# Kernel optimization log

Measured on AMD Instinct MI355X. Metric: run time of the kernel, lower is better.

## Reference

```python
import jax, jax.numpy as jnp
import numpy as np

N_MOLS = 2048
DEPTH = 4

def _graph_conv(fatoms, fbonds, agraph, bgraph, Wi, Wh, Wo, bo):
    # fbonds: [n_bonds, 88] -> nei_input_h: [n_bonds, H]
    nei_input_h = fbonds @ Wi.T
    msg = jax.nn.relu(nei_input_h)
    for _ in range(DEPTH - 1):
        # gather neighbor bond messages [n_bonds, max_nei, H], sum over neighbors
        nei = msg[bgraph].sum(axis=1)
        msg = jax.nn.relu(nei_input_h + nei @ Wh.T)
    # aggregate bond messages into atoms: [n_atoms, max_nei, H] -> [n_atoms, H]
    atom_nei = msg[agraph].sum(axis=1)
    atom_in = jnp.concatenate([fatoms, atom_nei], axis=1)  # [n_atoms, 82+H]
    return jax.nn.relu(atom_in @ Wo.T + bo)

def _mol_embed(atom_h, mol_idx):
    return jax.ops.segment_sum(atom_h, mol_idx, num_segments=N_MOLS)

def setup_inputs() -> dict:
    key = jax.random.key(0)
    ks = jax.random.split(key, 24)
    n_atoms, n_bonds, max_nei, H = 100000, 200000, 10, 256
    d = {}
    d['fatoms_src'] = jax.random.normal(ks[0], (n_atoms, 82), jnp.float32)
    d['fbonds_src'] = jax.random.normal(ks[1], (n_bonds, 88), jnp.float32)
    d['agraph_src'] = jax.random.randint(ks[2], (n_atoms, max_nei), 0, n_bonds, jnp.int32)
    d['bgraph_src'] = jax.random.randint(ks[3], (n_bonds, max_nei), 0, n_bonds, jnp.int32)
    d['mol_idx_src'] = jnp.sort(jax.random.randint(ks[4], (n_atoms,), 0, N_MOLS, jnp.int32))
    d['fatoms_tgt'] = jax.random.normal(ks[5], (n_atoms, 82), jnp.float32)
    d['fbonds_tgt'] = jax.random.normal(ks[6], (n_bonds, 88), jnp.float32)
    d['agraph_tgt'] = jax.random.randint(ks[7], (n_atoms, max_nei), 0, n_bonds, jnp.int32)
    d['bgraph_tgt'] = jax.random.randint(ks[8], (n_bonds, max_nei), 0, n_bonds, jnp.int32)
    d['mol_idx_tgt'] = jnp.sort(jax.random.randint(ks[9], (n_atoms,), 0, N_MOLS, jnp.int32))
    s = 0.05
    d['Wi_s'] = jax.random.normal(ks[10], (H, 88), jnp.float32) * s
    d['Wh_s'] = jax.random.normal(ks[11], (H, H), jnp.float32) * s
    d['Wo_s'] = jax.random.normal(ks[12], (H, 82 + H), jnp.float32) * s
    d['bo_s'] = jax.random.normal(ks[13], (H,), jnp.float32) * s
    d['Wi_t'] = jax.random.normal(ks[14], (H, 88), jnp.float32) * s
    d['Wh_t'] = jax.random.normal(ks[15], (H, H), jnp.float32) * s
    d['Wo_t'] = jax.random.normal(ks[16], (H, 82 + H), jnp.float32) * s
    d['bo_t'] = jax.random.normal(ks[17], (H,), jnp.float32) * s
    d['Wrh'] = jax.random.normal(ks[18], (H, H), jnp.float32) * s
    d['brh'] = jax.random.normal(ks[19], (H,), jnp.float32) * s
    d['Wro'] = jax.random.normal(ks[20], (1, H), jnp.float32) * s
    d['bro'] = jax.random.normal(ks[21], (1,), jnp.float32) * s
    return d

def reference(fatoms_src, fbonds_src, agraph_src, bgraph_src, mol_idx_src,
              fatoms_tgt, fbonds_tgt, agraph_tgt, bgraph_tgt, mol_idx_tgt,
              Wi_s, Wh_s, Wo_s, bo_s, Wi_t, Wh_t, Wo_t, bo_t,
              Wrh, brh, Wro, bro):
    src_atom_h = _graph_conv(fatoms_src, fbonds_src, agraph_src, bgraph_src, Wi_s, Wh_s, Wo_s, bo_s)
    src_mol_h = _mol_embed(src_atom_h, mol_idx_src)
    tgt_atom_h = _graph_conv(fatoms_tgt, fbonds_tgt, agraph_tgt, bgraph_tgt, Wi_t, Wh_t, Wo_t, bo_t)
    tgt_mol_h = _mol_embed(tgt_atom_h, mol_idx_tgt)
    rxn_h = jax.nn.relu((tgt_mol_h - src_mol_h) @ Wrh.T + brh)
    return rxn_h @ Wro.T + bro  # [N_MOLS, 1]
```

## Files before the change

kernel.cpp:

```cpp
#include <hip/hip_runtime.h>

typedef _Float16 f16;
using f16x8 = __attribute__((ext_vector_type(8))) _Float16;
using f32x4 = __attribute__((ext_vector_type(4))) float;

#define H 256
#define NM 2048

__device__ __forceinline__ void gload_lds16(const f16* g, f16* lds)
{
    __builtin_amdgcn_global_load_lds(
        (const __attribute__((address_space(1))) void*)g,
        (__attribute__((address_space(3))) void*)lds, 16, 0, 0);
}

__device__ __forceinline__ void gemm_body(
    f16 (*Bs)[64],
    const float* __restrict__ A1, int lda1, int K1r,
    const f16*  __restrict__ W1,
    const f16*  __restrict__ A2,
    const f16*  __restrict__ W2,
    const float* __restrict__ bias, f16* __restrict__ C,
    int bm, int Mend)
{
    const int tid  = threadIdx.x;
    const int wave = tid >> 6, lane = tid & 63;
    const int lrow = lane & 15;
    const int kg   = lane >> 4;
    const int swz  = lrow & 7;
    const int glr  = lane >> 3;
    const int gsc  = (lane & 7) ^ glr;

    const int  myrow = bm + wave * 16 + lrow;
    const bool rowok = myrow < Mend;

    f32x4 acc[16];
    #pragma unroll
    for (int n = 0; n < 16; ++n) acc[n] = (f32x4){0.f, 0.f, 0.f, 0.f};

    f16x8 af2[8];
    if (A2 != nullptr) {
        #pragma unroll
        for (int t = 0; t < 8; ++t) {
            if (rowok)
                af2[t] = *(const f16x8*)(A2 + (size_t)myrow * H + kg * 8 + t * 32);
            else {
                #pragma unroll
                for (int e = 0; e < 8; ++e) af2[t][e] = (f16)0.f;
            }
        }
    }

    auto stageB = [&](const f16* W, int ldw, int k0) {
        #pragma unroll
        for (int q = 0; q < 8; ++q)
            gload_lds16(W + (size_t)(wave * 64 + q * 8 + glr) * ldw + k0 + gsc * 8,
                        &Bs[wave * 64 + q * 8][0]);
    };

    auto mfma_win = [&](f16x8 a0, f16x8 a1) {
        #pragma unroll
        for (int ks = 0; ks < 2; ++ks) {
            const int cb = ((ks * 4 + kg) ^ swz) * 8;
            const f16x8 av = ks ? a1 : a0;
            #pragma unroll
            for (int n = 0; n < 16; ++n) {
                f16x8 b = *(const f16x8*)&Bs[n * 16 + lrow][cb];
                acc[n] = __builtin_amdgcn_mfma_f32_16x16x32_f16(av, b, acc[n], 0, 0, 0);
            }
        }
    };

    if (A1 != nullptr) {
        #pragma unroll
        for (int w = 0; w < 2; ++w) {
            f16x8 a[2];
            #pragma unroll
            for (int c = 0; c < 2; ++c) {
                const int k0 = (w * 8 + c * 4 + kg) * 8;
                const float* sp = A1 + (size_t)myrow * lda1 + k0;
                f16 tmp[8];
                #pragma unroll
                for (int i = 0; i < 8; i += 2) {
                    float x = 0.f, y = 0.f;
                    if (rowok) {
                        if (k0 + i + 1 < K1r) { float2 v = *(const float2*)(sp + i); x = v.x; y = v.y; }
                        else if (k0 + i < K1r) { x = sp[i]; }
                    }
                    tmp[i] = (f16)x; tmp[i + 1] = (f16)y;
                }
                a[c] = *(const f16x8*)tmp;
            }
            stageB(W1, 128, w * 64);
            __syncthreads();
            mfma_win(a[0], a[1]);
            __syncthreads();
        }
    }

    if (A2 != nullptr) {
        #pragma unroll
        for (int w = 0; w < 4; ++w) {
            stageB(W2, H, w * 64);
            __syncthreads();
            mfma_win(af2[w * 2], af2[w * 2 + 1]);
            __syncthreads();
        }
    }

    #pragma unroll
    for (int n = 0; n < 16; ++n) {
        const int gc = n * 16 + lrow;
        const float bv = bias ? bias[gc] : 0.f;
        #pragma unroll
        for (int r = 0; r < 4; ++r) {
            const int gr = bm + wave * 16 + kg * 4 + r;
            if (gr < Mend) C[(size_t)gr * H + gc] = (f16)fmaxf(acc[n][r] + bv, 0.f);
        }
    }
}

__device__ __forceinline__ void gather_body(
    const f16* __restrict__ src, const int* __restrict__ idx,
    f16* __restrict__ dst, int row, int lane)
{
    const int* ip = idx + (size_t)row * 10;
    float s[8] = {};
    #pragma unroll
    for (int j = 0; j < 10; ++j) {
        int r = ip[j];
        float4 v = *((const float4*)(src + (size_t)r * H) + lane);
        const f16* pb = (const f16*)&v;
        #pragma unroll
        for (int e = 0; e < 8; ++e) s[e] += (float)pb[e];
    }
    f16 o[8];
    #pragma unroll
    for (int e = 0; e < 8; ++e) o[e] = (f16)s[e];
    *((float4*)(dst + (size_t)row * H) + lane) = *(const float4*)o;
}

__global__ __launch_bounds__(256, 4) void gemm_dense(
    const float* __restrict__ A1, int lda1, int K1r,
    const f16*  __restrict__ W1,
    const f16*  __restrict__ A2,
    const f16*  __restrict__ W2,
    const float* __restrict__ bias, f16* __restrict__ C,
    int row0, int Mend)
{
    __shared__ f16 Bs[256][64];
    gemm_body(Bs, A1, lda1, K1r, W1, A2, W2, bias, C, row0 + blockIdx.x * 64, Mend);
}

__global__ __launch_bounds__(256) void gather_sum10(
    const f16* __restrict__ src, const int* __restrict__ idx,
    f16* __restrict__ dst, int row0, int rend)
{
    int row = row0 + blockIdx.x * 8 + (threadIdx.x >> 5);
    if (row < rend) gather_body(src, idx, dst, row, threadIdx.x & 31);
}

__global__ __launch_bounds__(256, 4) void fused_step(
    const float* __restrict__ A1, int lda1, int K1r,
    const f16*  __restrict__ W1,
    const f16*  __restrict__ A2,
    const f16*  __restrict__ W2,
    const float* __restrict__ bias, f16* __restrict__ C,
    int g_row0, int g_Mend, int nge, int period,
    const f16* __restrict__ gsrc, const int* __restrict__ gidx,
    f16* __restrict__ gdst, int a_row0, int a_end)
{
    __shared__ f16 Bs[256][64];
    const int bid = blockIdx.x;
    const int q = bid / period, r = bid % period;
    if (r == 0 && q < nge) {
        gemm_body(Bs, A1, lda1, K1r, W1, A2, W2, bias, C, g_row0 + q * 64, g_Mend);
    } else {
        int ab = bid - min(q + 1, nge);
        int row = a_row0 + ab * 8 + (threadIdx.x >> 5);
        if (row < a_end) gather_body(gsrc, gidx, gdst, row, threadIdx.x & 31);
    }
}

__global__ __launch_bounds__(256) void convert_w(
    const float* __restrict__ src, int lds_, int koff, int kvalid,
    f16* __restrict__ dst, int Kd)
{
    int n = blockIdx.x;
    for (int k = threadIdx.x; k < Kd; k += 256) {
        float v = (k < kvalid) ? src[(size_t)n * lds_ + koff + k] : 0.f;
        dst[(size_t)n * Kd + k] = (f16)v;
    }
}

__global__ __launch_bounds__(256) void segsum(
    const f16* __restrict__ atom_h, const int* __restrict__ mol_idx,
    float* __restrict__ mol_h, int n_atoms)
{
    int m = blockIdx.x;
    int lo = 0, hi = n_atoms;
    while (lo < hi) { int mid = (lo + hi) >> 1; if (mol_idx[mid] < m) lo = mid + 1; else hi = mid; }
    int start = lo;
    hi = n_atoms;
    while (lo < hi) { int mid = (lo + hi) >> 1; if (mol_idx[mid] < m + 1) lo = mid + 1; else hi = mid; }
    int end = lo;
    int c = threadIdx.x;
    float s = 0.f;
    for (int a = start; a < end; ++a) s += (float)atom_h[(size_t)a * H + c];
    mol_h[(size_t)m * H + c] = s;
}

__global__ __launch_bounds__(256) void diff_kernel(
    const float* __restrict__ a, const float* __restrict__ b,
    f16* __restrict__ c, int n)
{
    int i = blockIdx.x * 256 + threadIdx.x;
    if (i < n) c[i] = (f16)(a[i] - b[i]);
}

__global__ __launch_bounds__(256) void final_dot(
    const f16* __restrict__ rxn, const float* __restrict__ Wro,
    const float* __restrict__ bro, float* __restrict__ out)
{
    int m = blockIdx.x;
    int t = threadIdx.x;
    float v = (float)rxn[(size_t)m * H + t] * Wro[t];
    #pragma unroll
    for (int off = 32; off; off >>= 1) v += __shfl_down(v, off, 64);
    __shared__ float red[4];
    if ((t & 63) == 0) red[t >> 6] = v;
    __syncthreads();
    if (t == 0) out[m] = red[0] + red[1] + red[2] + red[3] + bro[0];
}

static void run_graph(const float* fatoms, const float* fbonds, const int* agraph,
                      const int* bgraph, const int* mol_idx,
                      const f16* Wi16, const f16* Wh16, const f16* Wo1, const f16* Wo2,
                      const float* bo,
                      f16* bufA, f16* bufB, f16* bufY, bool overlap, float* molh,
                      int n_atoms, int n_bonds, hipStream_t stream)
{
    const float* nul_f = nullptr;
    const f16*   nul_h = nullptr;

    gemm_dense<<<(n_bonds + 63) / 64, 256, 0, stream>>>(
        fbonds, 88, 88, Wi16, nul_h, nul_h, nul_f, bufA, 0, n_bonds);
    f16* cur = bufA; f16* nxt = bufB;

    if (!overlap) {
        for (int it = 0; it < 3; ++it) {
            gather_sum10<<<(n_bonds + 7) / 8, 256, 0, stream>>>(cur, bgraph, nxt, 0, n_bonds);
            gemm_dense<<<(n_bonds + 63) / 64, 256, 0, stream>>>(
                fbonds, 88, 88, Wi16, nxt, Wh16, nul_f, cur, 0, n_bonds);
        }
        gather_sum10<<<(n_atoms + 7) / 8, 256, 0, stream>>>(cur, agraph, nxt, 0, n_atoms);
        gemm_dense<<<(n_atoms + 63) / 64, 256, 0, stream>>>(
            fatoms, 82, 82, Wo1, nxt, Wo2, bo, cur, 0, n_atoms);
        segsum<<<NM, 256, 0, stream>>>(cur, mol_idx, molh, n_atoms);
        return;
    }

    const int hb  = min((((n_bonds / 2) + 63) / 64) * 64, n_bonds);
    const int nge_b = hb / 64;
    const int nga_b = (n_bonds - hb + 7) / 8;
    const int tot_b = nge_b + nga_b;
    const int per_b = tot_b / nge_b;

    for (int it = 0; it < 3; ++it) {
        gather_sum10<<<(hb + 7) / 8, 256, 0, stream>>>(cur, bgraph, bufY, 0, hb);
        fused_step<<<tot_b, 256, 0, stream>>>(
            fbonds, 88, 88, Wi16, bufY, Wh16, nul_f, nxt, 0, hb, nge_b, per_b,
            cur, bgraph, bufY, hb, n_bonds);
        gemm_dense<<<(n_bonds - hb + 63) / 64, 256, 0, stream>>>(
            fbonds, 88, 88, Wi16, bufY, Wh16, nul_f, nxt, hb, n_bonds);
        f16* t = cur; cur = nxt; nxt = t;
    }

    const int ahb  = min((((n_atoms / 2) + 63) / 64) * 64, n_atoms);
    const int nge_a = ahb / 64;
    const int nga_a = (n_atoms - ahb + 7) / 8;
    const int tot_a = nge_a + nga_a;
    const int per_a = tot_a / nge_a;

    gather_sum10<<<(ahb + 7) / 8, 256, 0, stream>>>(cur, agraph, bufY, 0, ahb);
    fused_step<<<tot_a, 256, 0, stream>>>(
        fatoms, 82, 82, Wo1, bufY, Wo2, bo, nxt, 0, ahb, nge_a, per_a,
        cur, agraph, bufY, ahb, n_atoms);
    gemm_dense<<<(n_atoms - ahb + 63) / 64, 256, 0, stream>>>(
        fatoms, 82, 82, Wo1, bufY, Wo2, bo, nxt, ahb, n_atoms);
    segsum<<<NM, 256, 0, stream>>>(nxt, mol_idx, molh, n_atoms);
}

extern "C" void kernel_launch(void* const* d_in, const int* in_sizes, int n_in,
                              void* d_out, int out_size, void* d_ws, size_t ws_size,
                              hipStream_t stream)
{
    const float* fatoms_src = (const float*)d_in[0];
    const float* fbonds_src = (const float*)d_in[1];
    const int*   agraph_src = (const int*)d_in[2];
    const int*   bgraph_src = (const int*)d_in[3];
    const int*   mol_idx_src= (const int*)d_in[4];
    const float* fatoms_tgt = (const float*)d_in[5];
    const float* fbonds_tgt = (const float*)d_in[6];
    const int*   agraph_tgt = (const int*)d_in[7];
    const int*   bgraph_tgt = (const int*)d_in[8];
    const int*   mol_idx_tgt= (const int*)d_in[9];
    const float* Wi_s = (const float*)d_in[10];
    const float* Wh_s = (const float*)d_in[11];
    const float* Wo_s = (const float*)d_in[12];
    const float* bo_s = (const float*)d_in[13];
    const float* Wi_t = (const float*)d_in[14];
    const float* Wh_t = (const float*)d_in[15];
    const float* Wo_t = (const float*)d_in[16];
    const float* bo_t = (const float*)d_in[17];
    const float* Wrh  = (const float*)d_in[18];
    const float* brh  = (const float*)d_in[19];
    const float* Wro  = (const float*)d_in[20];
    const float* bro  = (const float*)d_in[21];

    const int n_atoms = in_sizes[0] / 82;
    const int n_bonds = in_sizes[1] / 88;

    const size_t bondB = (size_t)n_bonds * H * sizeof(f16);
    const size_t tailB = 2 * (size_t)NM * H * 4 + 2 * (size_t)NM * H * 2
                       + 4 * (256 * 128 * 2) + 5 * (256 * 256 * 2)
                       + 32 * 256;
    const bool overlap = ws_size >= 3 * bondB + tailB;

    char* ws = (char*)d_ws;
    size_t off = 0;
    auto alloc = [&](size_t bytes) { size_t o = off; off = (off + bytes + 255) & ~(size_t)255; return o; };
    f16*   bufA = (f16*)(ws + alloc(bondB));
    f16*   bufB = (f16*)(ws + alloc(bondB));
    f16*   bufY = overlap ? (f16*)(ws + alloc(bondB)) : nullptr;
    float* molS = (float*)(ws + alloc((size_t)NM * H * 4));
    float* molT = (float*)(ws + alloc((size_t)NM * H * 4));
    f16*   dbuf = (f16*)(ws + alloc((size_t)NM * H * 2));
    f16*   rxn  = (f16*)(ws + alloc((size_t)NM * H * 2));
    f16* Wi16_s = (f16*)(ws + alloc(256 * 128 * 2));
    f16* Wh16_s = (f16*)(ws + alloc(256 * 256 * 2));
    f16* Wo1_s  = (f16*)(ws + alloc(256 * 128 * 2));
    f16* Wo2_s  = (f16*)(ws + alloc(256 * 256 * 2));
    f16* Wi16_t = (f16*)(ws + alloc(256 * 128 * 2));
    f16* Wh16_t = (f16*)(ws + alloc(256 * 256 * 2));
    f16* Wo1_t  = (f16*)(ws + alloc(256 * 128 * 2));
    f16* Wo2_t  = (f16*)(ws + alloc(256 * 256 * 2));
    f16* Wrh16  = (f16*)(ws + alloc(256 * 256 * 2));

    convert_w<<<256, 256, 0, stream>>>(Wi_s,  88,  0,  88, Wi16_s, 128);
    convert_w<<<256, 256, 0, stream>>>(Wh_s, 256,  0, 256, Wh16_s, 256);
    convert_w<<<256, 256, 0, stream>>>(Wo_s, 338,  0,  82, Wo1_s, 128);
    convert_w<<<256, 256, 0, stream>>>(Wo_s, 338, 82, 256, Wo2_s, 256);
    convert_w<<<256, 256, 0, stream>>>(Wi_t,  88,  0,  88, Wi16_t, 128);
    convert_w<<<256, 256, 0, stream>>>(Wh_t, 256,  0, 256, Wh16_t, 256);
    convert_w<<<256, 256, 0, stream>>>(Wo_t, 338,  0,  82, Wo1_t, 128);
    convert_w<<<256, 256, 0, stream>>>(Wo_t, 338, 82, 256, Wo2_t, 256);
    convert_w<<<256, 256, 0, stream>>>(Wrh, 256,  0, 256, Wrh16, 256);

    run_graph(fatoms_src, fbonds_src, agraph_src, bgraph_src, mol_idx_src,
              Wi16_s, Wh16_s, Wo1_s, Wo2_s, bo_s,
              bufA, bufB, bufY, overlap, molS, n_atoms, n_bonds, stream);
    run_graph(fatoms_tgt, fbonds_tgt, agraph_tgt, bgraph_tgt, mol_idx_tgt,
              Wi16_t, Wh16_t, Wo1_t, Wo2_t, bo_t,
              bufA, bufB, bufY, overlap, molT, n_atoms, n_bonds, stream);

    diff_kernel<<<(NM * H + 255) / 256, 256, 0, stream>>>(molT, molS, dbuf, NM * H);
    gemm_dense<<<NM / 64, 256, 0, stream>>>(
        (const float*)nullptr, 0, 0, (const f16*)nullptr, dbuf, Wrh16,
        brh, rxn, 0, NM);
    final_dot<<<NM, 256, 0, stream>>>(rxn, Wro, bro, (float*)d_out);
}
```

Measured before the change: 2.323 ms.

## Pipeline gather and GEMM in four chunks, computing in place to drop third buffer

```diff
diff --git a/kernel.cpp b/kernel.cpp
--- a/kernel.cpp
+++ b/kernel.cpp
@@ -18,9 +18,9 @@
     f16 (*Bs)[64],
     const float* __restrict__ A1, int lda1, int K1r,
     const f16*  __restrict__ W1,
-    const f16*  __restrict__ A2,
+    const f16* A2,
     const f16*  __restrict__ W2,
-    const float* __restrict__ bias, f16* __restrict__ C,
+    const float* __restrict__ bias, f16* C,
     int bm, int Mend)
 {
     const int tid  = threadIdx.x;
@@ -143,9 +143,9 @@
 __global__ __launch_bounds__(256, 4) void gemm_dense(
     const float* __restrict__ A1, int lda1, int K1r,
     const f16*  __restrict__ W1,
-    const f16*  __restrict__ A2,
+    const f16* A2,
     const f16*  __restrict__ W2,
-    const float* __restrict__ bias, f16* __restrict__ C,
+    const float* __restrict__ bias, f16* C,
     int row0, int Mend)
 {
     __shared__ f16 Bs[256][64];
@@ -163,9 +163,9 @@
 __global__ __launch_bounds__(256, 4) void fused_step(
     const float* __restrict__ A1, int lda1, int K1r,
     const f16*  __restrict__ W1,
-    const f16*  __restrict__ A2,
+    const f16* A2,
     const f16*  __restrict__ W2,
-    const float* __restrict__ bias, f16* __restrict__ C,
+    const float* __restrict__ bias, f16* C,
     int g_row0, int g_Mend, int nge, int period,
     const f16* __restrict__ gsrc, const int* __restrict__ gidx,
     f16* __restrict__ gdst, int a_row0, int a_end)
@@ -233,11 +233,41 @@
     if (t == 0) out[m] = red[0] + red[1] + red[2] + red[3] + bro[0];
 }
 
+static void stage_pipelined(const float* A1, int lda1, int K1r, const f16* W1,
+                            const f16* src_buf, const int* idx, const f16* W2,
+                            const float* bias, f16* ybuf, int n,
+                            hipStream_t stream)
+{
+    const int NC = 4;
+    const int CS = (((n + NC - 1) / NC + 63) / 64) * 64;
+    auto lo = [&](int c) { return min(c * CS, n); };
+    auto hi = [&](int c) { return min((c + 1) * CS, n); };
+
+    gather_sum10<<<(hi(0) - lo(0) + 7) / 8, 256, 0, stream>>>(src_buf, idx, ybuf, lo(0), hi(0));
+
+    for (int c = 0; c < NC; ++c) {
+        const int gs = lo(c), ge = hi(c);
+        const int as = lo(c + 1), ae = hi(c + 1);
+        const int nge = (ge - gs + 63) / 64;
+        if (ae > as) {
+            const int nga = (ae - as + 7) / 8;
+            const int tot = nge + nga;
+            const int per = tot / nge > 0 ? tot / nge : 1;
+            fused_step<<<tot, 256, 0, stream>>>(
+                A1, lda1, K1r, W1, ybuf, W2, bias, ybuf,
+                gs, ge, nge, per, src_buf, idx, ybuf, as, ae);
+        } else {
+            gemm_dense<<<nge, 256, 0, stream>>>(
+                A1, lda1, K1r, W1, ybuf, W2, bias, ybuf, gs, ge);
+        }
+    }
+}
+
 static void run_graph(const float* fatoms, const float* fbonds, const int* agraph,
                       const int* bgraph, const int* mol_idx,
                       const f16* Wi16, const f16* Wh16, const f16* Wo1, const f16* Wo2,
                       const float* bo,
-                      f16* bufA, f16* bufB, f16* bufY, bool overlap, float* molh,
+                      f16* bufA, f16* bufB, float* molh,
                       int n_atoms, int n_bonds, hipStream_t stream)
 {
     const float* nul_f = nullptr;
@@ -247,47 +277,13 @@
         fbonds, 88, 88, Wi16, nul_h, nul_h, nul_f, bufA, 0, n_bonds);
     f16* cur = bufA; f16* nxt = bufB;
 
-    if (!overlap) {
-        for (int it = 0; it < 3; ++it) {
-            gather_sum10<<<(n_bonds + 7) / 8, 256, 0, stream>>>(cur, bgraph, nxt, 0, n_bonds);
-            gemm_dense<<<(n_bonds + 63) / 64, 256, 0, stream>>>(
-                fbonds, 88, 88, Wi16, nxt, Wh16, nul_f, cur, 0, n_bonds);
-        }
-        gather_sum10<<<(n_atoms + 7) / 8, 256, 0, stream>>>(cur, agraph, nxt, 0, n_atoms);
-        gemm_dense<<<(n_atoms + 63) / 64, 256, 0, stream>>>(
-            fatoms, 82, 82, Wo1, nxt, Wo2, bo, cur, 0, n_atoms);
-        segsum<<<NM, 256, 0, stream>>>(cur, mol_idx, molh, n_atoms);
-        return;
-    }
-
-    const int hb  = min((((n_bonds / 2) + 63) / 64) * 64, n_bonds);
-    const int nge_b = hb / 64;
-    const int nga_b = (n_bonds - hb + 7) / 8;
-    const int tot_b = nge_b + nga_b;
-    const int per_b = tot_b / nge_b;
-
     for (int it = 0; it < 3; ++it) {
-        gather_sum10<<<(hb + 7) / 8, 256, 0, stream>>>(cur, bgraph, bufY, 0, hb);
-        fused_step<<<tot_b, 256, 0, stream>>>(
-            fbonds, 88, 88, Wi16, bufY, Wh16, nul_f, nxt, 0, hb, nge_b, per_b,
-            cur, bgraph, bufY, hb, n_bonds);
-        gemm_dense<<<(n_bonds - hb + 63) / 64, 256, 0, stream>>>(
-            fbonds, 88, 88, Wi16, bufY, Wh16, nul_f, nxt, hb, n_bonds);
+        stage_pipelined(fbonds, 88, 88, Wi16, cur, bgraph, Wh16,
+                        nul_f, nxt, n_bonds, stream);
         f16* t = cur; cur = nxt; nxt = t;
     }
-
-    const int ahb  = min((((n_atoms / 2) + 63) / 64) * 64, n_atoms);
-    const int nge_a = ahb / 64;
-    const int nga_a = (n_atoms - ahb + 7) / 8;
-    const int tot_a = nge_a + nga_a;
-    const int per_a = tot_a / nge_a;
-
-    gather_sum10<<<(ahb + 7) / 8, 256, 0, stream>>>(cur, agraph, bufY, 0, ahb);
-    fused_step<<<tot_a, 256, 0, stream>>>(
-        fatoms, 82, 82, Wo1, bufY, Wo2, bo, nxt, 0, ahb, nge_a, per_a,
-        cur, agraph, bufY, ahb, n_atoms);
-    gemm_dense<<<(n_atoms - ahb + 63) / 64, 256, 0, stream>>>(
-        fatoms, 82, 82, Wo1, bufY, Wo2, bo, nxt, ahb, n_atoms);
+    stage_pipelined(fatoms, 82, 82, Wo1, cur, agraph, Wo2,
+                    bo, nxt, n_atoms, stream);
     segsum<<<NM, 256, 0, stream>>>(nxt, mol_idx, molh, n_atoms);
 }
 
@@ -321,18 +317,11 @@
     const int n_atoms = in_sizes[0] / 82;
     const int n_bonds = in_sizes[1] / 88;
 
-    const size_t bondB = (size_t)n_bonds * H * sizeof(f16);
-    const size_t tailB = 2 * (size_t)NM * H * 4 + 2 * (size_t)NM * H * 2
-                       + 4 * (256 * 128 * 2) + 5 * (256 * 256 * 2)
-                       + 32 * 256;
-    const bool overlap = ws_size >= 3 * bondB + tailB;
-
     char* ws = (char*)d_ws;
     size_t off = 0;
     auto alloc = [&](size_t bytes) { size_t o = off; off = (off + bytes + 255) & ~(size_t)255; return o; };
-    f16*   bufA = (f16*)(ws + alloc(bondB));
-    f16*   bufB = (f16*)(ws + alloc(bondB));
-    f16*   bufY = overlap ? (f16*)(ws + alloc(bondB)) : nullptr;
+    f16*   bufA = (f16*)(ws + alloc((size_t)n_bonds * H * 2));
+    f16*   bufB = (f16*)(ws + alloc((size_t)n_bonds * H * 2));
     float* molS = (float*)(ws + alloc((size_t)NM * H * 4));
     float* molT = (float*)(ws + alloc((size_t)NM * H * 4));
     f16*   dbuf = (f16*)(ws + alloc((size_t)NM * H * 2));
@@ -359,10 +348,10 @@
 
     run_graph(fatoms_src, fbonds_src, agraph_src, bgraph_src, mol_idx_src,
               Wi16_s, Wh16_s, Wo1_s, Wo2_s, bo_s,
-              bufA, bufB, bufY, overlap, molS, n_atoms, n_bonds, stream);
+              bufA, bufB, molS, n_atoms, n_bonds, stream);
     run_graph(fatoms_tgt, fbonds_tgt, agraph_tgt, bgraph_tgt, mol_idx_tgt,
               Wi16_t, Wh16_t, Wo1_t, Wo2_t, bo_t,
-              bufA, bufB, bufY, overlap, molT, n_atoms, n_bonds, stream);
+              bufA, bufB, molT, n_atoms, n_bonds, stream);
 
     diff_kernel<<<(NM * H + 255) / 256, 256, 0, stream>>>(molT, molS, dbuf, NM * H);
     gemm_dense<<<NM / 64, 256, 0, stream>>>(
```

New measurement: 3.577 ms. 54.0% more time.
